# Optimization experiments

Hardware: AMD Instinct MI355X
Metric: run time of the kernel (lower is better)

## Reference

```python
import jax, jax.numpy as jnp
import numpy as np

R, E, N, B = 64, 100000, 1000000, 4

def setup_inputs() -> dict:
    key = jax.random.key(0)
    k1, k2, k3 = jax.random.split(key, 3)
    p = jax.random.normal(k1, (R,), dtype=jnp.float32)
    edges = jax.random.randint(k2, (R, E, 2), 0, N, dtype=jnp.int64)
    x = jax.random.normal(k3, (B, N), dtype=jnp.float32)
    return {"p": p, "edges": edges, "x": x}

def reference(p, edges, x):
    # _A = sum_r p[r] * (A_r + A_r^T), with A_r[u,v] += 1 per edge (duplicates sum,
    # matching scipy csr_matrix construction). y = x @ _A, i.e.
    # y[b, j] = sum over edges (u,v) of relation r: p[r]*x[b,u] into j=v and p[r]*x[b,v] into j=u.
    num_entities = x.shape[1]
    e = edges.shape[1]
    src = edges[..., 0].reshape(-1)            # [R*E]
    dst = edges[..., 1].reshape(-1)            # [R*E]
    w = jnp.repeat(p, e)                       # [R*E] per-edge relation weight
    # include inverse edges
    srcs = jnp.concatenate([src, dst])         # [2RE]
    dsts = jnp.concatenate([dst, src])         # [2RE]
    ww = jnp.concatenate([w, w])               # [2RE]
    vals = x[:, srcs].T * ww[:, None]          # [2RE, B] gathered & weighted messages
    y = jax.ops.segment_sum(vals, dsts, num_segments=num_entities).T  # [B, N]
    return y
```

## Files before the change

### kernel.cpp

```cpp
#include <hip/hip_runtime.h>
#include <hip/hip_fp16.h>


constexpr int  R_   = 64;
constexpr long E_   = 100000;
constexpr int  N_   = 1000000;
constexpr long RE_  = (long)R_ * E_;
constexpr long M2_  = 2 * RE_;
constexpr int  BSH  = 11;
constexpr int  BUCKET = 1 << BSH;
constexpr int  NB   = (N_ + BUCKET - 1) >> BSH;
constexpr int  NBP  = 512;
constexpr int  SH   = 19;
constexpr int  NC2  = NB * 2;
constexpr int  EPB  = 4096;
constexpr int  HB   = (int)((RE_ + EPB - 1) / EPB);
constexpr int  RPB  = 5632;

__global__ __launch_bounds__(256) void k_transpose_h(const float* __restrict__ x,
                                                     uint2* __restrict__ xTh) {
    int i = blockIdx.x * 256 + threadIdx.x;
    if (i < N_) {
        __half2 a = __floats2half2_rn(x[i],           x[(long)N_ + i]);
        __half2 b = __floats2half2_rn(x[2L * N_ + i], x[3L * N_ + i]);
        xTh[i] = make_uint2(__builtin_bit_cast(unsigned, a),
                            __builtin_bit_cast(unsigned, b));
    }
}

__global__ __launch_bounds__(256) void k_hist(const unsigned long long* __restrict__ edges8,
                                              int* __restrict__ g_bcnt) {
    __shared__ int lc[NC2];
    for (int i = threadIdx.x; i < NC2; i += 256) lc[i] = 0;
    __syncthreads();
    long k0 = (long)blockIdx.x * EPB;
    int lim = (int)min((long)EPB, RE_ - k0);
    for (int i = threadIdx.x; i < lim; i += 256) {
        unsigned long long ev = __builtin_nontemporal_load(edges8 + k0 + i);
        int u = (int)(unsigned)ev, v = (int)(ev >> 32);
        atomicAdd(&lc[((v >> BSH) << 1) | (u >> SH)], 1);
        atomicAdd(&lc[((u >> BSH) << 1) | (v >> SH)], 1);
    }
    __syncthreads();
    for (int c = threadIdx.x; c < NC2; c += 256)
        g_bcnt[(size_t)c * HB + blockIdx.x] = lc[c];
}

__global__ __launch_bounds__(256) void k_cellscan(const int* __restrict__ g_bcnt,
                                                  int* __restrict__ g_bbase,
                                                  int* __restrict__ ctot) {
    __shared__ int sA[256], sB[256];
    const int c = blockIdx.x, t = threadIdx.x;
    int run = 0;
    for (int chunk = 0; chunk < HB; chunk += 256) {
        int b = chunk + t;
        int v = (b < HB) ? g_bcnt[(size_t)c * HB + b] : 0;
        sA[t] = v;
        __syncthreads();
        int* A = sA; int* B = sB;
        for (int off = 1; off < 256; off <<= 1) {
            int xv = A[t];
            if (t >= off) xv += A[t - off];
            B[t] = xv;
            __syncthreads();
            int* tmp = A; A = B; B = tmp;
        }
        int incl = A[t];
        if (b < HB) g_bbase[(size_t)c * HB + b] = run + incl - v;
        run += A[255];
        __syncthreads();
    }
    if (t == 0) ctot[c] = run;
}

__global__ __launch_bounds__(1024) void k_scan(const int* __restrict__ ctot,
                                               int* __restrict__ cbase) {
    __shared__ int sA[1024], sB[1024];
    int t = threadIdx.x;
    sA[t] = (t < NC2) ? ctot[t] : 0;
    __syncthreads();
    int* A = sA; int* B = sB;
    for (int off = 1; off < 1024; off <<= 1) {
        int xv = A[t];
        if (t >= off) xv += A[t - off];
        B[t] = xv;
        __syncthreads();
        int* tmp = A; A = B; B = tmp;
    }
    if (t < NC2) cbase[t] = t ? A[t - 1] : 0;
    if (t == 0) cbase[NC2] = A[NC2 - 1];
}

__global__ __launch_bounds__(1024) void k_bin_h(const unsigned long long* __restrict__ edges8,
                                                const float* __restrict__ p,
                                                const uint2* __restrict__ xTh,
                                                const int* __restrict__ g_bcnt,
                                                const int* __restrict__ g_bbase,
                                                const int* __restrict__ cbase,
                                                const int h,
                                                unsigned short* __restrict__ g_dst,
                                                unsigned long long* __restrict__ g_pay) {
    __shared__ int                l_dst[RPB];
    __shared__ unsigned long long l_pay[RPB];
    __shared__ int sA[NBP], sB[NBP];
    __shared__ int excl[NB], cur[NB], gbase[NB];
    __shared__ float pl[R_];
    __shared__ int s_total;
    const int t = threadIdx.x, blk = blockIdx.x;

    if (t < NBP) {
        int v = 0;
        if (t < NB) {
            size_t idx = (size_t)((t << 1) | h) * HB + blk;
            v = g_bcnt[idx];
            gbase[t] = cbase[(t << 1) | h] + g_bbase[idx];
        }
        sA[t] = v;
    }
    if (t < R_) pl[t] = p[t];
    __syncthreads();
    int* A = sA; int* B = sB;
    for (int off = 1; off < NBP; off <<= 1) {
        if (t < NBP) { int v = A[t]; if (t >= off) v += A[t - off]; B[t] = v; }
        __syncthreads();
        int* tmp = A; A = B; B = tmp;
    }
    if (t < NB) { int e = t ? A[t - 1] : 0; excl[t] = e; cur[t] = e; }
    if (t == 0) s_total = A[NB - 1];
    __syncthreads();

    const long k0 = (long)blk * EPB;
    const int lim = (int)min((long)EPB, RE_ - k0);
    #pragma unroll
    for (int j = 0; j < EPB / 1024; ++j) {
        int i = t + j * 1024;
        if (i < lim) {
            unsigned long long ev = __builtin_nontemporal_load(edges8 + k0 + i);
            int u = (int)(unsigned)ev, v = (int)(ev >> 32);
            float w = pl[(unsigned)(k0 + i) / (unsigned)E_];
            if ((u >> SH) == h) {
                uint2 xv = xTh[u];
                __half2 h0 = __builtin_bit_cast(__half2, xv.x);
                __half2 h1 = __builtin_bit_cast(__half2, xv.y);
                unsigned plo = __builtin_bit_cast(unsigned,
                    __floats2half2_rn(w * __low2float(h0), w * __high2float(h0)));
                unsigned phi = __builtin_bit_cast(unsigned,
                    __floats2half2_rn(w * __low2float(h1), w * __high2float(h1)));
                int pos = atomicAdd(&cur[v >> BSH], 1);
                if (pos < RPB) {
                    l_dst[pos] = v;
                    l_pay[pos] = ((unsigned long long)phi << 32) | plo;
                }
            }
            if ((v >> SH) == h) {
                uint2 xv = xTh[v];
                __half2 h0 = __builtin_bit_cast(__half2, xv.x);
                __half2 h1 = __builtin_bit_cast(__half2, xv.y);
                unsigned plo = __builtin_bit_cast(unsigned,
                    __floats2half2_rn(w * __low2float(h0), w * __high2float(h0)));
                unsigned phi = __builtin_bit_cast(unsigned,
                    __floats2half2_rn(w * __low2float(h1), w * __high2float(h1)));
                int pos = atomicAdd(&cur[u >> BSH], 1);
                if (pos < RPB) {
                    l_dst[pos] = u;
                    l_pay[pos] = ((unsigned long long)phi << 32) | plo;
                }
            }
        }
    }
    __syncthreads();
    const int total = s_total;
    for (int s = t; s < total; s += 1024) {
        int dst = l_dst[s];
        int d = dst >> BSH;
        int pos = gbase[d] + (s - excl[d]);
        g_dst[pos] = (unsigned short)(dst & (BUCKET - 1));
        __builtin_nontemporal_store(l_pay[s], g_pay + pos);
    }
}

__global__ __launch_bounds__(1024) void k_accum(const unsigned short* __restrict__ g_dst,
                                                const unsigned long long* __restrict__ g_pay,
                                                const int* __restrict__ cbase,
                                                float* __restrict__ y) {
    __shared__ unsigned long long accA[BUCKET];
    __shared__ unsigned long long accB[BUCKET];
    const int t = threadIdx.x, b = blockIdx.x;
    for (int i = t; i < BUCKET; i += 1024) { accA[i] = 0ull; accB[i] = 0ull; }
    __syncthreads();
    const int lo = cbase[2 * b], hi = cbase[2 * b + 2];
    for (int i = lo + t; i < hi; i += 1024) {
        int dl = (int)g_dst[i];
        unsigned long long pay = __builtin_nontemporal_load(g_pay + i);
        __half2 h01 = __builtin_bit_cast(__half2, (unsigned)pay);
        __half2 h23 = __builtin_bit_cast(__half2, (unsigned)(pay >> 32));
        float f0 = fminf(fmaxf(__low2float(h01),  -31.f), 31.f);
        float f1 = fminf(fmaxf(__high2float(h01), -31.f), 31.f);
        float f2 = fminf(fmaxf(__low2float(h23),  -31.f), 31.f);
        float f3 = fminf(fmaxf(__high2float(h23), -31.f), 31.f);
        unsigned e0 = (unsigned)(__float2int_rn(f0 * 65536.f) + (1 << 21));
        unsigned e1 = (unsigned)(__float2int_rn(f1 * 65536.f) + (1 << 21));
        unsigned e2 = (unsigned)(__float2int_rn(f2 * 65536.f) + (1 << 21));
        unsigned e3 = (unsigned)(__float2int_rn(f3 * 65536.f) + (1 << 21));
        unsigned long long va = (unsigned long long)e0
                              | ((unsigned long long)e1 << 28)
                              | (1ull << 56);
        unsigned long long vb = (unsigned long long)e2
                              | ((unsigned long long)e3 << 28);
        atomicAdd(&accA[dl], va);
        atomicAdd(&accB[dl], vb);
    }
    __syncthreads();
    const int base_e = b << BSH;
    for (int j = t; j < BUCKET; j += 1024) {
        int i = base_e + j;
        if (i < N_) {
            unsigned long long a = accA[j], bb = accB[j];
            long deg  = (long)(a >> 56);
            long bias = deg << 21;
            long c0 = (long)(a & 0xFFFFFFFull) - bias;
            long c1 = (long)((a >> 28) & 0xFFFFFFFull) - bias;
            long c2 = (long)(bb & 0xFFFFFFFull) - bias;
            long c3 = (long)((bb >> 28) & 0xFFFFFFFull) - bias;
            const float sc = 1.f / 65536.f;
            y[i]            = (float)c0 * sc;
            y[(long)N_ + i] = (float)c1 * sc;
            y[2L * N_ + i]  = (float)c2 * sc;
            y[3L * N_ + i]  = (float)c3 * sc;
        }
    }
}

__global__ __launch_bounds__(256) void k_scatter_direct(const int2* __restrict__ edges,
                                                        const float* __restrict__ p,
                                                        const float* __restrict__ x,
                                                        float* __restrict__ y) {
    const long stride = (long)gridDim.x * blockDim.x;
    for (long k = (long)blockIdx.x * blockDim.x + threadIdx.x; k < RE_; k += stride) {
        int2 e = edges[k];
        float w = p[(int)(k / E_)];
        #pragma unroll
        for (int b = 0; b < 4; ++b) {
            float xu = x[(long)b * N_ + e.x];
            float xv = x[(long)b * N_ + e.y];
            atomicAdd(&y[(long)b * N_ + e.y], w * xu);
            atomicAdd(&y[(long)b * N_ + e.x], w * xv);
        }
    }
}

extern "C" void kernel_launch(void* const* d_in, const int* in_sizes, int n_in,
                              void* d_out, int out_size, void* d_ws, size_t ws_size,
                              hipStream_t stream) {
    const float* p     = (const float*)d_in[0];
    const int*   edges = (const int*)d_in[1];
    const float* x     = (const float*)d_in[2];
    float*       y     = (float*)d_out;

    const size_t xTh_bytes   = (size_t)N_ * 8;
    const size_t pay_bytes   = (size_t)M2_ * 8;
    const size_t dst_bytes   = (size_t)M2_ * 2;
    const size_t bcnt_bytes  = (size_t)NC2 * HB * 4;
    const size_t ctot_bytes  = (size_t)NC2 * 4;
    const size_t cbase_bytes = (size_t)(NC2 + 1) * 4;
    const size_t need = xTh_bytes + pay_bytes + dst_bytes + 2 * bcnt_bytes
                      + ctot_bytes + cbase_bytes;

    if (ws_size >= need) {
        char* ws = (char*)d_ws;
        uint2* xTh = (uint2*)ws;                       ws += xTh_bytes;
        unsigned long long* g_pay = (unsigned long long*)ws;  ws += pay_bytes;
        int* g_bcnt  = (int*)ws;                       ws += bcnt_bytes;
        int* g_bbase = (int*)ws;                       ws += bcnt_bytes;
        int* ctot    = (int*)ws;                       ws += ctot_bytes;
        int* cbase   = (int*)ws;                       ws += cbase_bytes;
        unsigned short* g_dst = (unsigned short*)ws;

        k_transpose_h<<<(N_ + 255) / 256, 256, 0, stream>>>(x, xTh);
        k_hist<<<HB, 256, 0, stream>>>((const unsigned long long*)edges, g_bcnt);
        k_cellscan<<<NC2, 256, 0, stream>>>(g_bcnt, g_bbase, ctot);
        k_scan<<<1, 1024, 0, stream>>>(ctot, cbase);
        k_bin_h<<<HB, 1024, 0, stream>>>((const unsigned long long*)edges, p,
                                         (const uint2*)xTh, g_bcnt, g_bbase,
                                         cbase, 0, g_dst, g_pay);
        k_bin_h<<<HB, 1024, 0, stream>>>((const unsigned long long*)edges, p,
                                         (const uint2*)xTh, g_bcnt, g_bbase,
                                         cbase, 1, g_dst, g_pay);
        k_accum<<<NB, 1024, 0, stream>>>((const unsigned short*)g_dst,
                                         (const unsigned long long*)g_pay, cbase, y);
    } else {
        hipMemsetAsync(y, 0, (size_t)out_size * sizeof(float), stream);
        k_scatter_direct<<<8192, 256, 0, stream>>>((const int2*)edges, p, x, y);
    }
}
```

Baseline: 287.7 us.

## Two-pass binning: sort messages by source bucket before gathering x

Replaces the two half-range binning passes with a pipeline that first bins edges by source bucket, packing dst and relation index, and allocates slabs with atomic tails. A message-build pass then gathers x rows in source-local order, weights them, and rebins by destination for the accumulator. This is meant to make the random xTh gathers cache-friendly and to drop the per-block prefix-scan bookkeeping. The cost is an extra round trip of intermediate buffers through global memory, a binary search per message, and slab order that depends on atomics, so summation order is nondeterministic.

```diff
diff --git a/kernel.cpp b/kernel.cpp
--- a/kernel.cpp
+++ b/kernel.cpp
@@ -11,11 +11,11 @@
 constexpr int  BUCKET = 1 << BSH;
 constexpr int  NB   = (N_ + BUCKET - 1) >> BSH;
 constexpr int  NBP  = 512;
-constexpr int  SH   = 19;
-constexpr int  NC2  = NB * 2;
 constexpr int  EPB  = 4096;
 constexpr int  HB   = (int)((RE_ + EPB - 1) / EPB);
-constexpr int  RPB  = 5632;
+constexpr int  RPB  = 2 * EPB;
+constexpr int  MCH  = 8192;
+constexpr int  MBB  = (int)((M2_ + MCH - 1) / MCH);
 
 __global__ __launch_bounds__(256) void k_transpose_h(const float* __restrict__ x,
                                                      uint2* __restrict__ xTh) {
@@ -30,94 +30,68 @@
 
 __global__ __launch_bounds__(256) void k_hist(const unsigned long long* __restrict__ edges8,
                                               int* __restrict__ g_bcnt) {
-    __shared__ int lc[NC2];
-    for (int i = threadIdx.x; i < NC2; i += 256) lc[i] = 0;
+    __shared__ int lc[NB];
+    for (int i = threadIdx.x; i < NB; i += 256) lc[i] = 0;
     __syncthreads();
     long k0 = (long)blockIdx.x * EPB;
     int lim = (int)min((long)EPB, RE_ - k0);
     for (int i = threadIdx.x; i < lim; i += 256) {
         unsigned long long ev = __builtin_nontemporal_load(edges8 + k0 + i);
-        int u = (int)(unsigned)ev, v = (int)(ev >> 32);
-        atomicAdd(&lc[((v >> BSH) << 1) | (u >> SH)], 1);
-        atomicAdd(&lc[((u >> BSH) << 1) | (v >> SH)], 1);
-    }
-    __syncthreads();
-    for (int c = threadIdx.x; c < NC2; c += 256)
+        unsigned u = (unsigned)ev, v = (unsigned)(ev >> 32);
+        atomicAdd(&lc[u >> BSH], 1);
+        atomicAdd(&lc[v >> BSH], 1);
+    }
+    __syncthreads();
+    for (int c = threadIdx.x; c < NB; c += 256)
         g_bcnt[(size_t)c * HB + blockIdx.x] = lc[c];
 }
 
-__global__ __launch_bounds__(256) void k_cellscan(const int* __restrict__ g_bcnt,
-                                                  int* __restrict__ g_bbase,
-                                                  int* __restrict__ ctot) {
-    __shared__ int sA[256], sB[256];
+__global__ __launch_bounds__(256) void k_colsum(const int* __restrict__ g_bcnt,
+                                                int* __restrict__ ctot) {
+    __shared__ int red[256];
     const int c = blockIdx.x, t = threadIdx.x;
-    int run = 0;
-    for (int chunk = 0; chunk < HB; chunk += 256) {
-        int b = chunk + t;
-        int v = (b < HB) ? g_bcnt[(size_t)c * HB + b] : 0;
-        sA[t] = v;
+    int s = 0;
+    for (int b = t; b < HB; b += 256) s += g_bcnt[(size_t)c * HB + b];
+    red[t] = s;
+    __syncthreads();
+    for (int off = 128; off > 0; off >>= 1) {
+        if (t < off) red[t] += red[t + off];
         __syncthreads();
-        int* A = sA; int* B = sB;
-        for (int off = 1; off < 256; off <<= 1) {
-            int xv = A[t];
-            if (t >= off) xv += A[t - off];
-            B[t] = xv;
-            __syncthreads();
-            int* tmp = A; A = B; B = tmp;
-        }
-        int incl = A[t];
-        if (b < HB) g_bbase[(size_t)c * HB + b] = run + incl - v;
-        run += A[255];
-        __syncthreads();
-    }
-    if (t == 0) ctot[c] = run;
-}
-
-__global__ __launch_bounds__(1024) void k_scan(const int* __restrict__ ctot,
-                                               int* __restrict__ cbase) {
-    __shared__ int sA[1024], sB[1024];
+    }
+    if (t == 0) ctot[c] = red[0];
+}
+
+__global__ __launch_bounds__(512) void k_scan(const int* __restrict__ ctot,
+                                              int* __restrict__ cbase,
+                                              int* __restrict__ tailA,
+                                              int* __restrict__ tailB) {
+    __shared__ int sA[NBP], sB[NBP];
     int t = threadIdx.x;
-    sA[t] = (t < NC2) ? ctot[t] : 0;
+    sA[t] = (t < NB) ? ctot[t] : 0;
     __syncthreads();
     int* A = sA; int* B = sB;
-    for (int off = 1; off < 1024; off <<= 1) {
-        int xv = A[t];
-        if (t >= off) xv += A[t - off];
-        B[t] = xv;
+    for (int off = 1; off < NBP; off <<= 1) {
+        int v = A[t];
+        if (t >= off) v += A[t - off];
+        B[t] = v;
         __syncthreads();
         int* tmp = A; A = B; B = tmp;
     }
-    if (t < NC2) cbase[t] = t ? A[t - 1] : 0;
-    if (t == 0) cbase[NC2] = A[NC2 - 1];
-}
-
-__global__ __launch_bounds__(1024) void k_bin_h(const unsigned long long* __restrict__ edges8,
-                                                const float* __restrict__ p,
-                                                const uint2* __restrict__ xTh,
-                                                const int* __restrict__ g_bcnt,
-                                                const int* __restrict__ g_bbase,
-                                                const int* __restrict__ cbase,
-                                                const int h,
-                                                unsigned short* __restrict__ g_dst,
-                                                unsigned long long* __restrict__ g_pay) {
-    __shared__ int                l_dst[RPB];
-    __shared__ unsigned long long l_pay[RPB];
+    if (t < NB) { int e = t ? A[t - 1] : 0; cbase[t] = e; tailA[t] = e; tailB[t] = e; }
+    if (t == 0) cbase[NB] = A[NB - 1];
+}
+
+__global__ __launch_bounds__(1024) void k_srcbin(const unsigned long long* __restrict__ edges8,
+                                                 const int* __restrict__ g_bcnt,
+                                                 int* __restrict__ g_tailA,
+                                                 unsigned short* __restrict__ g_sl,
+                                                 unsigned* __restrict__ g_dr) {
+    __shared__ unsigned l_src[RPB];
+    __shared__ unsigned l_dr[RPB];
     __shared__ int sA[NBP], sB[NBP];
-    __shared__ int excl[NB], cur[NB], gbase[NB];
-    __shared__ float pl[R_];
-    __shared__ int s_total;
+    __shared__ int excl[NB], cur[NB], slab[NB];
     const int t = threadIdx.x, blk = blockIdx.x;
-
-    if (t < NBP) {
-        int v = 0;
-        if (t < NB) {
-            size_t idx = (size_t)((t << 1) | h) * HB + blk;
-            v = g_bcnt[idx];
-            gbase[t] = cbase[(t << 1) | h] + g_bbase[idx];
-        }
-        sA[t] = v;
-    }
-    if (t < R_) pl[t] = p[t];
+    if (t < NBP) sA[t] = (t < NB) ? g_bcnt[(size_t)t * HB + blk] : 0;
     __syncthreads();
     int* A = sA; int* B = sB;
     for (int off = 1; off < NBP; off <<= 1) {
@@ -126,56 +100,126 @@
         int* tmp = A; A = B; B = tmp;
     }
     if (t < NB) { int e = t ? A[t - 1] : 0; excl[t] = e; cur[t] = e; }
-    if (t == 0) s_total = A[NB - 1];
     __syncthreads();
 
     const long k0 = (long)blk * EPB;
     const int lim = (int)min((long)EPB, RE_ - k0);
+    const unsigned r0 = (unsigned)(k0 / E_);
+    const long bnd = (long)(r0 + 1) * E_;
     #pragma unroll
     for (int j = 0; j < EPB / 1024; ++j) {
         int i = t + j * 1024;
         if (i < lim) {
             unsigned long long ev = __builtin_nontemporal_load(edges8 + k0 + i);
-            int u = (int)(unsigned)ev, v = (int)(ev >> 32);
-            float w = pl[(unsigned)(k0 + i) / (unsigned)E_];
-            if ((u >> SH) == h) {
-                uint2 xv = xTh[u];
-                __half2 h0 = __builtin_bit_cast(__half2, xv.x);
-                __half2 h1 = __builtin_bit_cast(__half2, xv.y);
-                unsigned plo = __builtin_bit_cast(unsigned,
-                    __floats2half2_rn(w * __low2float(h0), w * __high2float(h0)));
-                unsigned phi = __builtin_bit_cast(unsigned,
-                    __floats2half2_rn(w * __low2float(h1), w * __high2float(h1)));
-                int pos = atomicAdd(&cur[v >> BSH], 1);
-                if (pos < RPB) {
-                    l_dst[pos] = v;
-                    l_pay[pos] = ((unsigned long long)phi << 32) | plo;
-                }
-            }
-            if ((v >> SH) == h) {
-                uint2 xv = xTh[v];
-                __half2 h0 = __builtin_bit_cast(__half2, xv.x);
-                __half2 h1 = __builtin_bit_cast(__half2, xv.y);
-                unsigned plo = __builtin_bit_cast(unsigned,
-                    __floats2half2_rn(w * __low2float(h0), w * __high2float(h0)));
-                unsigned phi = __builtin_bit_cast(unsigned,
-                    __floats2half2_rn(w * __low2float(h1), w * __high2float(h1)));
-                int pos = atomicAdd(&cur[u >> BSH], 1);
-                if (pos < RPB) {
-                    l_dst[pos] = u;
-                    l_pay[pos] = ((unsigned long long)phi << 32) | plo;
-                }
-            }
-        }
-    }
-    __syncthreads();
-    const int total = s_total;
+            unsigned u = (unsigned)ev, v = (unsigned)(ev >> 32);
+            unsigned r = (k0 + i >= bnd) ? r0 + 1 : r0;
+            int p1 = atomicAdd(&cur[u >> BSH], 1);
+            l_src[p1] = u;
+            l_dr[p1]  = v | (r << 20);
+            int p2 = atomicAdd(&cur[v >> BSH], 1);
+            l_src[p2] = v;
+            l_dr[p2]  = u | (r << 20);
+        }
+    }
+    __syncthreads();
+    for (int c = t; c < NB; c += 1024) {
+        int cnt = cur[c] - excl[c];
+        slab[c] = cnt ? atomicAdd(&g_tailA[c], cnt) : 0;
+    }
+    __syncthreads();
+    const int total = 2 * lim;
     for (int s = t; s < total; s += 1024) {
-        int dst = l_dst[s];
-        int d = dst >> BSH;
-        int pos = gbase[d] + (s - excl[d]);
-        g_dst[pos] = (unsigned short)(dst & (BUCKET - 1));
-        __builtin_nontemporal_store(l_pay[s], g_pay + pos);
+        unsigned src = l_src[s];
+        int c = (int)(src >> BSH);
+        int pos = slab[c] + (s - excl[c]);
+        g_sl[pos] = (unsigned short)(src & (BUCKET - 1));
+        __builtin_nontemporal_store(l_dr[s], g_dr + pos);
+    }
+}
+
+__global__ __launch_bounds__(1024) void k_msgbuild(const unsigned* __restrict__ g_dr,
+                                                   const unsigned short* __restrict__ g_sl,
+                                                   const int* __restrict__ cbase,
+                                                   int* __restrict__ g_tailB,
+                                                   const float* __restrict__ p,
+                                                   const uint2* __restrict__ xTh,
+                                                   unsigned short* __restrict__ g_dst2,
+                                                   unsigned long long* __restrict__ g_pay2) {
+    __shared__ unsigned l_dst[MCH];
+    __shared__ unsigned long long l_pay[MCH];
+    __shared__ int sA[NBP], sB[NBP];
+    __shared__ int excl[NB], cur[NB], slab[NB];
+    __shared__ int cbl[NBP];
+    __shared__ float pl[R_];
+    const int t = threadIdx.x, blk = blockIdx.x;
+    if (t < R_) pl[t] = p[t];
+    if (t < NBP) { sA[t] = 0; cbl[t] = (t <= NB) ? cbase[t] : 0x7fffffff; }
+    __syncthreads();
+
+    const long m0 = (long)blk * MCH;
+    const int lim = (int)min((long)MCH, M2_ - m0);
+    unsigned mdr[MCH / 1024];
+    unsigned msrc[MCH / 1024];
+    #pragma unroll
+    for (int j = 0; j < MCH / 1024; ++j) {
+        int k = t + j * 1024;
+        mdr[j] = 0; msrc[j] = 0;
+        if (k < lim) {
+            int m = (int)(m0 + k);
+            unsigned dr = __builtin_nontemporal_load(g_dr + m);
+            unsigned short sl = g_sl[m];
+            int lo = 0, hi = NB - 1;
+            while (lo < hi) { int mid = (lo + hi + 1) >> 1; if (cbl[mid] <= m) lo = mid; else hi = mid - 1; }
+            msrc[j] = ((unsigned)lo << BSH) | sl;
+            mdr[j] = dr;
+            atomicAdd(&sA[(dr & 0xFFFFFu) >> BSH], 1);
+        }
+    }
+    __syncthreads();
+    int* A = sA; int* B = sB;
+    for (int off = 1; off < NBP; off <<= 1) {
+        if (t < NBP) { int v = A[t]; if (t >= off) v += A[t - off]; B[t] = v; }
+        __syncthreads();
+        int* tmp = A; A = B; B = tmp;
+    }
+    if (t < NB) { int e = t ? A[t - 1] : 0; excl[t] = e; cur[t] = e; }
+    __syncthreads();
+    uint2 xg[MCH / 1024];
+    #pragma unroll
+    for (int j = 0; j < MCH / 1024; ++j) {
+        int k = t + j * 1024;
+        if (k < lim) xg[j] = xTh[msrc[j]];
+    }
+    #pragma unroll
+    for (int j = 0; j < MCH / 1024; ++j) {
+        int k = t + j * 1024;
+        if (k < lim) {
+            unsigned dr = mdr[j];
+            float w = pl[dr >> 20];
+            __half2 h0 = __builtin_bit_cast(__half2, xg[j].x);
+            __half2 h1 = __builtin_bit_cast(__half2, xg[j].y);
+            unsigned plo = __builtin_bit_cast(unsigned,
+                __floats2half2_rn(w * __low2float(h0), w * __high2float(h0)));
+            unsigned phi = __builtin_bit_cast(unsigned,
+                __floats2half2_rn(w * __low2float(h1), w * __high2float(h1)));
+            unsigned dst = dr & 0xFFFFFu;
+            int pos = atomicAdd(&cur[dst >> BSH], 1);
+            l_dst[pos] = dst;
+            l_pay[pos] = ((unsigned long long)phi << 32) | plo;
+        }
+    }
+    __syncthreads();
+    for (int c = t; c < NB; c += 1024) {
+        int cnt = cur[c] - excl[c];
+        slab[c] = cnt ? atomicAdd(&g_tailB[c], cnt) : 0;
+    }
+    __syncthreads();
+    for (int s = t; s < lim; s += 1024) {
+        unsigned dst = l_dst[s];
+        int c = (int)(dst >> BSH);
+        int pos = slab[c] + (s - excl[c]);
+        g_dst2[pos] = (unsigned short)(dst & (BUCKET - 1));
+        __builtin_nontemporal_store(l_pay[s], g_pay2 + pos);
     }
 }
 
@@ -188,7 +232,7 @@
     const int t = threadIdx.x, b = blockIdx.x;
     for (int i = t; i < BUCKET; i += 1024) { accA[i] = 0ull; accB[i] = 0ull; }
     __syncthreads();
-    const int lo = cbase[2 * b], hi = cbase[2 * b + 2];
+    const int lo = cbase[b], hi = cbase[b + 1];
     for (int i = lo + t; i < hi; i += 1024) {
         int dl = (int)g_dst[i];
         unsigned long long pay = __builtin_nontemporal_load(g_pay + i);
@@ -257,37 +301,43 @@
     const float* x     = (const float*)d_in[2];
     float*       y     = (float*)d_out;
 
+    const size_t pay_bytes   = (size_t)M2_ * 8;
+    const size_t dr_bytes    = (size_t)M2_ * 4;
     const size_t xTh_bytes   = (size_t)N_ * 8;
-    const size_t pay_bytes   = (size_t)M2_ * 8;
-    const size_t dst_bytes   = (size_t)M2_ * 2;
-    const size_t bcnt_bytes  = (size_t)NC2 * HB * 4;
-    const size_t ctot_bytes  = (size_t)NC2 * 4;
-    const size_t cbase_bytes = (size_t)(NC2 + 1) * 4;
-    const size_t need = xTh_bytes + pay_bytes + dst_bytes + 2 * bcnt_bytes
-                      + ctot_bytes + cbase_bytes;
+    const size_t bcnt_bytes  = (size_t)NB * HB * 4;
+    const size_t ctot_bytes  = (size_t)NBP * 4;
+    const size_t cbase_bytes = (size_t)(NB + 1) * 4;
+    const size_t tail_bytes  = (size_t)NB * 4;
+    const size_t sl_bytes    = (size_t)M2_ * 2;
+    const size_t dst2_bytes  = (size_t)M2_ * 2;
+    const size_t need = pay_bytes + dr_bytes + xTh_bytes + bcnt_bytes + ctot_bytes
+                      + cbase_bytes + 2 * tail_bytes + sl_bytes + dst2_bytes + 64;
 
     if (ws_size >= need) {
         char* ws = (char*)d_ws;
-        uint2* xTh = (uint2*)ws;                       ws += xTh_bytes;
-        unsigned long long* g_pay = (unsigned long long*)ws;  ws += pay_bytes;
-        int* g_bcnt  = (int*)ws;                       ws += bcnt_bytes;
-        int* g_bbase = (int*)ws;                       ws += bcnt_bytes;
-        int* ctot    = (int*)ws;                       ws += ctot_bytes;
-        int* cbase   = (int*)ws;                       ws += cbase_bytes;
-        unsigned short* g_dst = (unsigned short*)ws;
+        unsigned long long* g_pay2 = (unsigned long long*)ws;  ws += pay_bytes;
+        unsigned* g_dr = (unsigned*)ws;               ws += dr_bytes;
+        uint2*    xTh  = (uint2*)ws;                  ws += xTh_bytes;
+        int* g_bcnt = (int*)ws;                       ws += bcnt_bytes;
+        int* ctot   = (int*)ws;                       ws += ctot_bytes;
+        int* cbase  = (int*)ws;                       ws += cbase_bytes;
+        int* tailA  = (int*)ws;                       ws += tail_bytes;
+        int* tailB  = (int*)ws;                       ws += tail_bytes;
+        unsigned short* g_sl   = (unsigned short*)ws; ws += sl_bytes;
+        unsigned short* g_dst2 = (unsigned short*)ws;
 
         k_transpose_h<<<(N_ + 255) / 256, 256, 0, stream>>>(x, xTh);
         k_hist<<<HB, 256, 0, stream>>>((const unsigned long long*)edges, g_bcnt);
-        k_cellscan<<<NC2, 256, 0, stream>>>(g_bcnt, g_bbase, ctot);
-        k_scan<<<1, 1024, 0, stream>>>(ctot, cbase);
-        k_bin_h<<<HB, 1024, 0, stream>>>((const unsigned long long*)edges, p,
-                                         (const uint2*)xTh, g_bcnt, g_bbase,
-                                         cbase, 0, g_dst, g_pay);
-        k_bin_h<<<HB, 1024, 0, stream>>>((const unsigned long long*)edges, p,
-                                         (const uint2*)xTh, g_bcnt, g_bbase,
-                                         cbase, 1, g_dst, g_pay);
-        k_accum<<<NB, 1024, 0, stream>>>((const unsigned short*)g_dst,
-                                         (const unsigned long long*)g_pay, cbase, y);
+        k_colsum<<<NB, 256, 0, stream>>>(g_bcnt, ctot);
+        k_scan<<<1, 512, 0, stream>>>(ctot, cbase, tailA, tailB);
+        k_srcbin<<<HB, 1024, 0, stream>>>((const unsigned long long*)edges, g_bcnt,
+                                          tailA, g_sl, g_dr);
+        k_msgbuild<<<MBB, 1024, 0, stream>>>((const unsigned*)g_dr,
+                                             (const unsigned short*)g_sl,
+                                             cbase, tailB, p, (const uint2*)xTh,
+                                             g_dst2, g_pay2);
+        k_accum<<<NB, 1024, 0, stream>>>((const unsigned short*)g_dst2,
+                                         (const unsigned long long*)g_pay2, cbase, y);
     } else {
         hipMemsetAsync(y, 0, (size_t)out_size * sizeof(float), stream);
         k_scatter_direct<<<8192, 256, 0, stream>>>((const int2*)edges, p, x, y);
```

After: 283.3 us. Within noise of the previous version (-1.5%).
